# Optimization experiments

Measured on AMD Instinct MI355X. Metric: run time of the kernel, lower is better.

The kernel has to match this reference:

```python
import jax, jax.numpy as jnp
import numpy as np

EPS = 1e-5

def causal_conv1d(x, w, b, groups=1):
    # x: [B,C,L], w: [O, C//groups, K]; left-pad K-1 => causal, length preserved
    k = w.shape[-1]
    x = jnp.pad(x, ((0, 0), (0, 0), (k - 1, 0)))
    y = jax.lax.conv_general_dilated(x, w, (1,), 'VALID',
        dimension_numbers=('NCH', 'OIH', 'NCH'), feature_group_count=groups)
    return y + b[None, :, None]

def bn_eval(x, g, b):
    # BatchNorm1d eval with init running stats (mean=0, var=1)
    scale = g / jnp.sqrt(1.0 + EPS)
    return x * scale[None, :, None] + b[None, :, None]

def maxpool1d(x, k):
    B, C, L = x.shape
    return x.reshape(B, C, L // k, k).max(-1)

def mamba2_layer(u, Wi, cw, cb, dt_bias, A_log, Dh, norm_w, Wo):
    Bb, L, _ = u.shape
    H = dt_bias.shape[0]
    d_inner = norm_w.shape[0]
    P = d_inner // H
    conv_dim = cw.shape[0]
    N = (conv_dim - d_inner) // 2
    zxbcdt = u @ Wi                                   # [B,L,2*d_inner+2N+H]
    z = zxbcdt[..., :d_inner]
    xBC = zxbcdt[..., d_inner:d_inner + conv_dim]
    dt = zxbcdt[..., d_inner + conv_dim:]
    xBC = causal_conv1d(xBC.swapaxes(1, 2), cw[:, None, :], cb, groups=conv_dim)
    xBC = jax.nn.silu(xBC).swapaxes(1, 2)             # [B,L,conv_dim]
    xs = xBC[..., :d_inner].reshape(Bb, L, H, P)
    Bm = xBC[..., d_inner:d_inner + N]                # [B,L,N] (ngroups=1)
    Cm = xBC[..., d_inner + N:]                       # [B,L,N]
    dt = jax.nn.softplus(dt + dt_bias)                # [B,L,H]
    dA = jnp.exp(dt * (-jnp.exp(A_log)))              # [B,L,H]
    dtx = dt[..., None] * xs                          # [B,L,H,P]
    def step(h, inp):
        dA_t, dtx_t, B_t, C_t = inp
        h = h * dA_t[:, :, None, None] + dtx_t[..., None] * B_t[:, None, None, :]
        y = jnp.einsum('bhpn,bn->bhp', h, C_t)
        return h, y
    h0 = jnp.zeros((Bb, H, P, N), u.dtype)
    _, ys = jax.lax.scan(step, h0, (dA.swapaxes(0, 1), dtx.swapaxes(0, 1),
                                    Bm.swapaxes(0, 1), Cm.swapaxes(0, 1)))
    y = ys.swapaxes(0, 1) + Dh[None, None, :, None] * xs
    y = y.reshape(Bb, L, d_inner)
    y = y * jax.nn.silu(z)                            # gate then RMSNorm (norm_before_gate=False)
    y = y * jax.lax.rsqrt(jnp.mean(y * y, axis=-1, keepdims=True) + EPS) * norm_w
    return y @ Wo

def forward(x, idx, patch_w, patch_b, conv_w, conv_b, bn_g, bn_b,
            cls_token, pos_embed, Wi, cw, cb, dt_bias, A_log, Dh,
            norm_w, Wo, ln_g, ln_b, fc_w, fc_b):
    # PatchEmbed: Conv2d kernel (patch_size,1) on [B,1,patch_size,L] -> [B,E,L]
    h = jnp.einsum('bpl,ep->bel', x[:, 0], patch_w) + patch_b[None, :, None]
    # CausalCNN (eval mode: dropout = identity)
    h = jax.nn.relu(bn_eval(causal_conv1d(h, conv_w[0], conv_b[0]), bn_g[0], bn_b[0]))
    h = jax.nn.relu(bn_eval(causal_conv1d(h, conv_w[1], conv_b[1]), bn_g[1], bn_b[1]))
    h = maxpool1d(h, 3)
    h = jax.nn.relu(bn_eval(causal_conv1d(h, conv_w[2], conv_b[2]), bn_g[2], bn_b[2]))
    h = jax.nn.relu(bn_eval(causal_conv1d(h, conv_w[3], conv_b[3]), bn_g[3], bn_b[3]))
    h = maxpool1d(h, 2)
    h = h.swapaxes(1, 2)                              # [B, num_patches, E]
    h = h + pos_embed[:, 1:, :]
    cls = cls_token + pos_embed[:, :1, :]
    h = jnp.concatenate([jnp.broadcast_to(cls, (h.shape[0], 1, h.shape[2])), h], axis=1)
    def block(carry, p):
        return carry + mamba2_layer(carry, *p), None
    h, _ = jax.lax.scan(block, h, (Wi, cw, cb, dt_bias, A_log, Dh, norm_w, Wo))
    mu = h.mean(-1, keepdims=True)
    var = ((h - mu) ** 2).mean(-1, keepdims=True)
    h = (h - mu) * jax.lax.rsqrt(var + EPS) * ln_g + ln_b
    h = h[:, 1:, :]                                   # drop cls
    agg = idx // 6                                    # aggregate_idx
    mask = (jnp.arange(h.shape[1])[None, :] <= agg[:, None]).astype(h.dtype)
    pooled = (h * mask[..., None]).sum(1) / (agg + 1).astype(h.dtype)[:, None]
    return pooled @ fc_w + fc_b

def _sincos_pos_embed(E, L):
    pos = np.arange(L, dtype=np.float32)
    omega = 1.0 / 10000 ** (np.arange(E // 2, dtype=np.float32) / (E / 2.0))
    out = pos[:, None] * omega[None, :]
    emb = np.concatenate([np.sin(out), np.cos(out)], axis=1)
    emb = np.concatenate([np.zeros((1, E), np.float32), emb], axis=0)  # cls row
    return jnp.asarray(emb)[None]

def setup_inputs() -> dict:
    key = jax.random.key(0)
    ks = jax.random.split(key, 12)
    B, E, Lm, Psz = 16, 256, 12288, 8
    depth, H, N, d_inner, K = 8, 8, 128, 512, 4
    conv_dim = d_inner + 2 * N        # 768
    dproj = 2 * d_inner + 2 * N + H   # 1288
    NC = 100
    NP = Lm // 6                      # 2048 patches
    f32 = jnp.float32
    dt0 = jax.random.uniform(ks[2], (depth, H), f32, 0.001, 0.1)
    return dict(
        x=jax.random.normal(ks[0], (B, 1, Psz, Lm), f32),
        idx=jax.random.randint(ks[1], (B,), 0, Lm),
        patch_w=jax.random.normal(ks[3], (E, Psz), f32) * 0.1,
        patch_b=jnp.zeros((E,), f32),
        conv_w=jax.random.normal(ks[4], (4, E, E, 5), f32) * 0.02,
        conv_b=jnp.zeros((4, E), f32),
        bn_g=jnp.ones((4, E), f32), bn_b=jnp.zeros((4, E), f32),
        cls_token=jax.random.normal(ks[5], (1, 1, E), f32) * 0.02,
        pos_embed=_sincos_pos_embed(E, NP),
        Wi=jax.random.normal(ks[6], (depth, E, dproj), f32) * 0.06,
        cw=jax.random.normal(ks[7], (depth, conv_dim, K), f32) * 0.2,
        cb=jnp.zeros((depth, conv_dim), f32),
        dt_bias=dt0 + jnp.log(-jnp.expm1(-dt0)),  # inverse softplus of dt
        A_log=jnp.log(jax.random.uniform(ks[8], (depth, H), f32, 1.0, 16.0)),
        Dh=jnp.ones((depth, H), f32),
        norm_w=jnp.ones((depth, d_inner), f32),
        Wo=jax.random.normal(ks[9], (depth, d_inner, E), f32) * 0.04,
        ln_g=jnp.ones((E,), f32), ln_b=jnp.zeros((E,), f32),
        fc_w=jax.random.normal(ks[10], (E, NC), f32) * 0.05,
        fc_b=jnp.zeros((NC,), f32),
    )

def reference(x, idx, patch_w, patch_b, conv_w, conv_b, bn_g, bn_b,
              cls_token, pos_embed, Wi, cw, cb, dt_bias, A_log, Dh,
              norm_w, Wo, ln_g, ln_b, fc_w, fc_b):
    return forward(x, idx, patch_w, patch_b, conv_w, conv_b, bn_g, bn_b,
                   cls_token, pos_embed, Wi, cw, cb, dt_bias, A_log, Dh,
                   norm_w, Wo, ln_g, ln_b, fc_w, fc_b)
```

## Files before the change

kernel.cpp:

```cpp
#include <hip/hip_runtime.h>
#include <cstdint>
#include <cstddef>

#define EPSF 1e-5f

typedef unsigned short u16;
typedef __attribute__((ext_vector_type(8))) short short8v;
typedef __attribute__((ext_vector_type(4))) float f32x4;

static __device__ __forceinline__ u16 f2bf(float f) {
  union { float f; unsigned u; } v; v.f = f;
  unsigned r = v.u + 0x7fffu + ((v.u >> 16) & 1u);
  return (u16)(r >> 16);
}
static __device__ __forceinline__ float bf2f(u16 h) {
  union { unsigned u; float f; } v; v.u = ((unsigned)h) << 16;
  return v.f;
}

__global__ void k_wconv(const float* __restrict__ src, u16* __restrict__ dst) {
  int i = blockIdx.x * 256 + threadIdx.x;
  if (i >= 4 * 256 * 256 * 5) return;
  int k = i % 5, r = i / 5;
  int ci = r & 255; r >>= 8;
  int co = r & 255; int l = r >> 8;
  dst[(((size_t)l * 256 + co) * 5 + k) * 256 + ci] = f2bf(src[i]);
}
__global__ void k_wti(const float* __restrict__ src, u16* __restrict__ dst) {
  int i = blockIdx.x * 256 + threadIdx.x;
  if (i >= 8 * 1288 * 256) return;
  int k = i & 255; int r = i >> 8;
  int n = r % 1288; int l = r / 1288;
  dst[i] = f2bf(src[((size_t)l * 256 + k) * 1288 + n]);
}
__global__ void k_wto(const float* __restrict__ src, u16* __restrict__ dst) {
  int i = blockIdx.x * 256 + threadIdx.x;
  if (i >= 8 * 256 * 512) return;
  int k = i & 511; int r = i >> 9;
  int n = r & 255; int l = r >> 8;
  dst[i] = f2bf(src[((size_t)l * 512 + k) * 256 + n]);
}

__global__ __launch_bounds__(256) void k_patchm(const float* __restrict__ x, const float* __restrict__ pw,
                                                const float* __restrict__ pb, u16* __restrict__ outb) {
  __shared__ float xs[8][64];
  const int l0 = blockIdx.x * 64;
  const int b = blockIdx.y;
  const int tid = threadIdx.x;
  const float* xb = x + (size_t)b * 8 * 12288;
  for (int q = tid; q < 512; q += 256) {
    int p = q >> 6, ll = q & 63;
    xs[p][ll] = xb[(size_t)p * 12288 + l0 + ll];
  }
  __syncthreads();
  float pwr[8];
#pragma unroll
  for (int p = 0; p < 8; ++p) pwr[p] = pw[tid * 8 + p];
  const float bias = pb[tid];
  u16* ob = outb + ((size_t)b * 12288 + l0) * 256 + tid;
  for (int ll = 0; ll < 64; ++ll) {
    float acc = bias;
#pragma unroll
    for (int p = 0; p < 8; ++p) acc += xs[p][ll] * pwr[p];
    ob[(size_t)ll * 256] = f2bf(acc);
  }
}

template <int P2>
__global__ __launch_bounds__(256) void k_convm(const u16* __restrict__ in, const u16* __restrict__ wbf,
                                               const float* __restrict__ cbias, const float* __restrict__ bng,
                                               const float* __restrict__ bnb, u16* __restrict__ outb, int L) {
  __shared__ u16 Xs[132 * 40];
  __shared__ u16 Ws[64 * 168];
  const int l0 = blockIdx.x * 128;
  const int co0 = blockIdx.y * 64;
  const int b = blockIdx.z;
  const int tid = threadIdx.x;
  const int w = tid >> 6, l = tid & 63;
  const int mhalf = (w >> 1) * 64, nhalf = (w & 1) * 32;
  const u16* inb = in + (size_t)b * L * 256;
  f32x4 acc[4][2] = {};
  for (int ci0 = 0; ci0 < 256; ci0 += 32) {
    __syncthreads();
    for (int q = tid; q < 528; q += 256) {
      int row = q >> 2, coff = (q & 3) * 8;
      int gl = l0 - 4 + row;
      short8v v = {};
      if (gl >= 0) v = *(const short8v*)(inb + (size_t)gl * 256 + ci0 + coff);
      *(short8v*)(Xs + row * 40 + coff) = v;
    }
    for (int q = tid; q < 1280; q += 256) {
      int co = q / 20, rem = q % 20, k = rem >> 2, coff = (rem & 3) * 8;
      *(short8v*)(Ws + co * 168 + k * 32 + coff) =
          *(const short8v*)(wbf + ((size_t)(co0 + co) * 5 + k) * 256 + ci0 + coff);
    }
    __syncthreads();
    const int koff = (l >> 4) * 8;
    const int arow = mhalf + (l & 15);
    const int bro0 = (nhalf + (l & 15)) * 168;
    const int bro1 = (nhalf + 16 + (l & 15)) * 168;
#pragma unroll
    for (int k = 0; k < 5; ++k) {
      short8v b0 = *(const short8v*)(Ws + bro0 + k * 32 + koff);
      short8v b1 = *(const short8v*)(Ws + bro1 + k * 32 + koff);
#pragma unroll
      for (int mi = 0; mi < 4; ++mi) {
        short8v a = *(const short8v*)(Xs + (arow + mi * 16 + k) * 40 + koff);
        acc[mi][0] = __builtin_amdgcn_mfma_f32_16x16x32_bf16(a, b0, acc[mi][0], 0, 0, 0);
        acc[mi][1] = __builtin_amdgcn_mfma_f32_16x16x32_bf16(a, b1, acc[mi][1], 0, 0, 0);
      }
    }
  }
  const float scn = rsqrtf(1.f + EPSF);
  if constexpr (!P2) {
    u16* outbb = outb + (size_t)b * L * 256;
#pragma unroll
    for (int ni = 0; ni < 2; ++ni) {
      int co = co0 + nhalf + ni * 16 + (l & 15);
      float alpha = bng[co] * scn;
      float beta = cbias[co] * alpha + bnb[co];
#pragma unroll
      for (int mi = 0; mi < 4; ++mi)
#pragma unroll
        for (int r = 0; r < 4; ++r) {
          int row = l0 + mhalf + mi * 16 + (l >> 4) * 4 + r;
          float v = acc[mi][ni][r] * alpha + beta;
          outbb[(size_t)row * 256 + co] = f2bf(fmaxf(v, 0.f));
        }
    }
  } else {
    const int Lo = L >> 1;
    u16* outbb = outb + (size_t)b * Lo * 256;
#pragma unroll
    for (int ni = 0; ni < 2; ++ni) {
      int co = co0 + nhalf + ni * 16 + (l & 15);
      float alpha = bng[co] * scn;
      float beta = cbias[co] * alpha + bnb[co];
#pragma unroll
      for (int mi = 0; mi < 4; ++mi) {
        int base = l0 + mhalf + mi * 16 + (l >> 4) * 4;
        float vv[4];
#pragma unroll
        for (int r = 0; r < 4; ++r) vv[r] = fmaxf(acc[mi][ni][r] * alpha + beta, 0.f);
#pragma unroll
        for (int pr = 0; pr < 2; ++pr) {
          float m2 = fmaxf(vv[2 * pr], vv[2 * pr + 1]);
          int orow = (base >> 1) + pr;
          outbb[(size_t)orow * 256 + co] = f2bf(m2);
        }
      }
    }
  }
}

__global__ void k_mpb(const u16* __restrict__ in, u16* __restrict__ out, int Lout, int kp, size_t total) {
  size_t i = (size_t)blockIdx.x * 256 + threadIdx.x;
  if (i >= total) return;
  size_t c = i & 255;
  size_t rest = i >> 8;
  size_t lo = rest % (size_t)Lout;
  size_t b = rest / (size_t)Lout;
  const u16* p = in + (b * (size_t)Lout * kp + lo * kp) * 256 + c;
  float m = bf2f(p[0]);
  for (int j = 1; j < kp; ++j) m = fmaxf(m, bf2f(p[(size_t)j * 256]));
  out[i] = f2bf(m);
}

__global__ __launch_bounds__(256) void k_asmb(const u16* __restrict__ in, const float* __restrict__ pos,
                                              const float* __restrict__ cls, float* __restrict__ uc,
                                              u16* __restrict__ ubc) {
  int t = blockIdx.x;
  int b = blockIdx.y;
  int e = threadIdx.x;
  float v;
  if (t == 0)
    v = cls[e] + pos[e];
  else
    v = bf2f(in[((size_t)b * 2048 + (t - 1)) * 256 + e]) + pos[(size_t)t * 256 + e];
  size_t o = ((size_t)b * 2049 + t) * 256 + e;
  uc[o] = v;
  ubc[o] = f2bf(v);
}

template <int MODE>
__global__ __launch_bounds__(256) void k_gemmm(const u16* __restrict__ A, const u16* __restrict__ BT,
                                               u16* __restrict__ OB, float* __restrict__ DT,
                                               float* __restrict__ C, u16* __restrict__ ubf,
                                               int M, int N, int K) {
  __shared__ u16 As[128 * 40];
  __shared__ u16 Bs[64 * 40];
  const int n0 = blockIdx.x * 64;
  const int m0 = blockIdx.y * 128;
  const int tid = threadIdx.x;
  const int w = tid >> 6, l = tid & 63;
  const int mhalf = (w >> 1) * 64, nhalf = (w & 1) * 32;
  f32x4 acc[4][2] = {};
  for (int k0 = 0; k0 < K; k0 += 32) {
    __syncthreads();
    for (int q = tid; q < 512; q += 256) {
      int row = q >> 2, koff = (q & 3) * 8;
      short8v v = {};
      if (m0 + row < M) v = *(const short8v*)(A + (size_t)(m0 + row) * K + k0 + koff);
      *(short8v*)(As + row * 40 + koff) = v;
    }
    {
      int row = tid >> 2, koff = (tid & 3) * 8;
      short8v v = {};
      if (n0 + row < N) v = *(const short8v*)(BT + (size_t)(n0 + row) * K + k0 + koff);
      *(short8v*)(Bs + row * 40 + koff) = v;
    }
    __syncthreads();
    const int koff = (l >> 4) * 8;
    short8v b0 = *(const short8v*)(Bs + (nhalf + (l & 15)) * 40 + koff);
    short8v b1 = *(const short8v*)(Bs + (nhalf + 16 + (l & 15)) * 40 + koff);
#pragma unroll
    for (int mi = 0; mi < 4; ++mi) {
      short8v a = *(const short8v*)(As + (mhalf + mi * 16 + (l & 15)) * 40 + koff);
      acc[mi][0] = __builtin_amdgcn_mfma_f32_16x16x32_bf16(a, b0, acc[mi][0], 0, 0, 0);
      acc[mi][1] = __builtin_amdgcn_mfma_f32_16x16x32_bf16(a, b1, acc[mi][1], 0, 0, 0);
    }
  }
#pragma unroll
  for (int mi = 0; mi < 4; ++mi)
#pragma unroll
    for (int r = 0; r < 4; ++r) {
      int m = m0 + mhalf + mi * 16 + (l >> 4) * 4 + r;
      if (m >= M) continue;
#pragma unroll
      for (int ni = 0; ni < 2; ++ni) {
        int n = n0 + nhalf + ni * 16 + (l & 15);
        if (n >= N) continue;
        float v = acc[mi][ni][r];
        if constexpr (MODE == 0) {
          if (n < 1280) OB[(size_t)m * 1280 + n] = f2bf(v);
          else DT[(size_t)m * 8 + (n - 1280)] = v;
        } else {
          float vv = C[(size_t)m * N + n] + v;
          C[(size_t)m * N + n] = vv;
          ubf[(size_t)m * N + n] = f2bf(vv);
        }
      }
    }
}

__global__ __launch_bounds__(256) void k_dw(const u16* __restrict__ zxb, const float* __restrict__ dtr,
                                            const float* __restrict__ cw, const float* __restrict__ cb,
                                            const float* __restrict__ dtbias, const float* __restrict__ al,
                                            u16* __restrict__ xBCb, float* __restrict__ dtb,
                                            float* __restrict__ ldb) {
  const int bx = blockIdx.x;
  const int t0 = blockIdx.y * 16;
  const int b = blockIdx.z;
  if (bx == 3) {
    int h = threadIdx.x & 7, ro = threadIdx.x >> 3;
    if (ro < 16) {
      int r = t0 + ro;
      if (r < 2049) {
        float v = dtr[((size_t)b * 2049 + r) * 8 + h] + dtbias[h];
        float d = (v > 20.f) ? v : log1pf(expf(v));
        size_t o = ((size_t)b * 2049 + r) * 8 + h;
        dtb[o] = d;
        ldb[o] = -expf(al[h]) * d;
      }
    }
    return;
  }
  int c = bx * 256 + threadIdx.x;
  const u16* col = zxb + ((size_t)b * 2049) * 1280 + 512 + c;
  float cw0 = cw[c * 4 + 0], cw1 = cw[c * 4 + 1], cw2 = cw[c * 4 + 2], cw3 = cw[c * 4 + 3];
  const float bias = cb[c];
  float w0 = 0.f, w1 = 0.f, w2 = 0.f;
  if (t0 - 3 >= 0) w0 = bf2f(col[(size_t)(t0 - 3) * 1280]);
  if (t0 - 2 >= 0) w1 = bf2f(col[(size_t)(t0 - 2) * 1280]);
  if (t0 - 1 >= 0) w2 = bf2f(col[(size_t)(t0 - 1) * 1280]);
  int tend = t0 + 16; if (tend > 2049) tend = 2049;
  u16* ob = xBCb + ((size_t)b * 2049) * 768 + c;
  for (int t = t0; t < tend; ++t) {
    float v = bf2f(col[(size_t)t * 1280]);
    float acc = bias + w0 * cw0 + w1 * cw1 + w2 * cw2 + v * cw3;
    float sig = 1.f / (1.f + expf(-acc));
    ob[(size_t)t * 768] = f2bf(acc * sig);
    w0 = w1; w1 = w2; w2 = v;
  }
}

__global__ __launch_bounds__(256) void k_ssd_intra(const u16* __restrict__ xBCb,
                                                   const float* __restrict__ dtg,
                                                   const float* __restrict__ ldg,
                                                   u16* __restrict__ ybuf,
                                                   u16* __restrict__ sc,
                                                   float* __restrict__ dtot) {
  const int L = 2049;
  const int c = blockIdx.x, h = blockIdx.y, b = blockIdx.z;
  const int tid = threadIdx.x;
  const int w = tid >> 6, l = tid & 63;
  const int t0 = c * 128;
  int qc = L - t0; if (qc > 128) qc = 128;

  __shared__ u16 R1[128 * 136];
  __shared__ u16 R2[128 * 136];
  __shared__ float dt_s[128], Lc_s[128];

  const u16* xb = xBCb + ((size_t)b * L) * 768;

  if (tid < 64) {
    int i2 = tid * 2;
    float a0 = 0.f, a1 = 0.f, d0 = 0.f, d1 = 0.f;
    if (i2 < qc) { size_t r = ((size_t)b * L + t0 + i2) * 8 + h; a0 = ldg[r]; d0 = dtg[r]; }
    if (i2 + 1 < qc) { size_t r = ((size_t)b * L + t0 + i2 + 1) * 8 + h; a1 = ldg[r]; d1 = dtg[r]; }
    dt_s[i2] = d0; dt_s[i2 + 1] = d1;
    float v = a0 + a1;
#pragma unroll
    for (int dlt = 1; dlt < 64; dlt <<= 1) {
      float t = __shfl_up(v, dlt, 64);
      if (tid >= dlt) v += t;
    }
    Lc_s[i2 + 1] = v;
    Lc_s[i2] = v - a1;
  }

  for (int q = tid; q < 2048; q += 256) {
    int row = q >> 4, off = (q & 15) * 8;
    short8v vb = {}, vc = {};
    if (row < qc) {
      const u16* src = xb + (size_t)(t0 + row) * 768;
      vb = *(const short8v*)(src + 512 + off);
      vc = *(const short8v*)(src + 640 + off);
    }
    *(short8v*)(R1 + row * 136 + off) = vb;
    *(short8v*)(R2 + row * 136 + off) = vc;
  }
  __syncthreads();

  const int wm = (w >> 1) * 64, wn = (w & 1) * 64;
  f32x4 g[4][4] = {};
  const bool skipG = (wm < wn);
  if (!skipG) {
#pragma unroll
    for (int ks = 0; ks < 4; ++ks) {
      const int koff = ks * 32 + (l >> 4) * 8;
      short8v bf[4];
#pragma unroll
      for (int ni = 0; ni < 4; ++ni)
        bf[ni] = *(const short8v*)(R1 + (wn + ni * 16 + (l & 15)) * 136 + koff);
#pragma unroll
      for (int mi = 0; mi < 4; ++mi) {
        short8v a = *(const short8v*)(R2 + (wm + mi * 16 + (l & 15)) * 136 + koff);
#pragma unroll
        for (int ni = 0; ni < 4; ++ni)
          g[mi][ni] = __builtin_amdgcn_mfma_f32_16x16x32_bf16(a, bf[ni], g[mi][ni], 0, 0, 0);
      }
    }
  }
  __syncthreads();

#pragma unroll
  for (int mi = 0; mi < 4; ++mi)
#pragma unroll
    for (int r = 0; r < 4; ++r) {
      int t = wm + mi * 16 + (l >> 4) * 4 + r;
      float lct = Lc_s[t];
#pragma unroll
      for (int ni = 0; ni < 4; ++ni) {
        int s = wn + ni * 16 + (l & 15);
        float v = 0.f;
        if (s <= t) v = __expf(lct - Lc_s[s]) * dt_s[s] * g[mi][ni][r];
        R2[t * 136 + s] = f2bf(v);
      }
    }
  for (int q = tid; q < 1024; q += 256) {
    int s = q >> 3, pv = (q & 7) * 8;
    short8v v = {};
    if (s < qc) v = *(const short8v*)(xb + (size_t)(t0 + s) * 768 + h * 64 + pv);
#pragma unroll
    for (int j = 0; j < 8; ++j) R1[(pv + j) * 136 + s] = (u16)v[j];
  }
  if (tid == 0) dtot[((size_t)b * 8 + h) * 17 + c] = __expf(Lc_s[qc - 1]);
  __syncthreads();

  {
    const int wmy = (w >> 1) * 64, wny = (w & 1) * 32;
    f32x4 ya[4][2] = {};
#pragma unroll
    for (int ks = 0; ks < 4; ++ks) {
      const int koff = ks * 32 + (l >> 4) * 8;
      short8v b0 = *(const short8v*)(R1 + (wny + (l & 15)) * 136 + koff);
      short8v b1 = *(const short8v*)(R1 + (wny + 16 + (l & 15)) * 136 + koff);
#pragma unroll
      for (int mi = 0; mi < 4; ++mi) {
        short8v a = *(const short8v*)(R2 + (wmy + mi * 16 + (l & 15)) * 136 + koff);
        ya[mi][0] = __builtin_amdgcn_mfma_f32_16x16x32_bf16(a, b0, ya[mi][0], 0, 0, 0);
        ya[mi][1] = __builtin_amdgcn_mfma_f32_16x16x32_bf16(a, b1, ya[mi][1], 0, 0, 0);
      }
    }
    u16* yb = ybuf + ((size_t)b * L + t0) * 512 + h * 64;
#pragma unroll
    for (int mi = 0; mi < 4; ++mi)
#pragma unroll
      for (int r = 0; r < 4; ++r) {
        int t = wmy + mi * 16 + (l >> 4) * 4 + r;
        if (t >= qc) continue;
#pragma unroll
        for (int ni = 0; ni < 2; ++ni) {
          int p = wny + ni * 16 + (l & 15);
          yb[(size_t)t * 512 + p] = f2bf(ya[mi][ni][r]);
        }
      }
  }
  __syncthreads();

  {
    const float Lend = Lc_s[qc - 1];
    for (int q = tid; q < 8192; q += 256) {
      int p = q >> 7, s = q & 127;
      float w2 = __expf(Lend - Lc_s[s]) * dt_s[s];
      R1[p * 136 + s] = f2bf(bf2f(R1[p * 136 + s]) * w2);
    }
    for (int q = tid; q < 2048; q += 256) {
      int s = q >> 4, nv = (q & 15) * 8;
      short8v v = {};
      if (s < qc) v = *(const short8v*)(xb + (size_t)(t0 + s) * 768 + 512 + nv);
#pragma unroll
      for (int j = 0; j < 8; ++j) R2[(nv + j) * 136 + s] = (u16)v[j];
    }
  }
  __syncthreads();

  {
    const int wms = (w & 1) * 32, wns = (w >> 1) * 64;
    f32x4 sa[2][4] = {};
#pragma unroll
    for (int ks = 0; ks < 4; ++ks) {
      const int koff = ks * 32 + (l >> 4) * 8;
      short8v a0 = *(const short8v*)(R1 + (wms + (l & 15)) * 136 + koff);
      short8v a1 = *(const short8v*)(R1 + (wms + 16 + (l & 15)) * 136 + koff);
#pragma unroll
      for (int ni = 0; ni < 4; ++ni) {
        short8v bb = *(const short8v*)(R2 + (wns + ni * 16 + (l & 15)) * 136 + koff);
        sa[0][ni] = __builtin_amdgcn_mfma_f32_16x16x32_bf16(a0, bb, sa[0][ni], 0, 0, 0);
        sa[1][ni] = __builtin_amdgcn_mfma_f32_16x16x32_bf16(a1, bb, sa[1][ni], 0, 0, 0);
      }
    }
    u16* scp = sc + (((size_t)b * 8 + h) * 17 + c) * 8192;
#pragma unroll
    for (int mi = 0; mi < 2; ++mi)
#pragma unroll
      for (int r = 0; r < 4; ++r) {
        int p = wms + mi * 16 + (l >> 4) * 4 + r;
#pragma unroll
        for (int ni = 0; ni < 4; ++ni) {
          int n = wns + ni * 16 + (l & 15);
          scp[p * 128 + n] = f2bf(sa[mi][ni][r]);
        }
      }
  }
}

__global__ __launch_bounds__(256) void k_ssd_scan(u16* __restrict__ sc, const float* __restrict__ dtot,
                                                  int nbh) {
  int gid = blockIdx.x * 256 + threadIdx.x;
  int bh = gid >> 13;
  if (bh >= nbh) return;
  int elem = gid & 8191;
  u16* base = sc + (size_t)bh * 17 * 8192 + elem;
  const float* dtp = dtot + (size_t)bh * 17;
  float hc = 0.f;
#pragma unroll
  for (int cc = 0; cc < 17; ++cc) {
    float D = dtp[cc];
    float v = bf2f(base[(size_t)cc * 8192]);
    base[(size_t)cc * 8192] = f2bf(hc);
    hc = hc * D + v;
  }
}

__global__ __launch_bounds__(256) void k_ssd_inter(const u16* __restrict__ xBCb,
                                                   const float* __restrict__ ldg,
                                                   const u16* __restrict__ sc,
                                                   const float* __restrict__ Dh,
                                                   u16* __restrict__ ybuf) {
  const int L = 2049;
  const int c = blockIdx.x, h = blockIdx.y, b = blockIdx.z;
  const int tid = threadIdx.x;
  const int w = tid >> 6, l = tid & 63;
  const int t0 = c * 128;
  int qc = L - t0; if (qc > 128) qc = 128;

  __shared__ u16 Cs[128 * 136];
  __shared__ u16 H0[64 * 136];
  __shared__ float Lc_s[128];

  const u16* xb = xBCb + ((size_t)b * L) * 768;

  if (tid < 64) {
    int i2 = tid * 2;
    float a0 = 0.f, a1 = 0.f;
    if (i2 < qc) a0 = ldg[((size_t)b * L + t0 + i2) * 8 + h];
    if (i2 + 1 < qc) a1 = ldg[((size_t)b * L + t0 + i2 + 1) * 8 + h];
    float v = a0 + a1;
#pragma unroll
    for (int dlt = 1; dlt < 64; dlt <<= 1) {
      float t = __shfl_up(v, dlt, 64);
      if (tid >= dlt) v += t;
    }
    Lc_s[i2 + 1] = v;
    Lc_s[i2] = v - a1;
  }
  for (int q = tid; q < 2048; q += 256) {
    int row = q >> 4, off = (q & 15) * 8;
    short8v vc = {};
    if (row < qc) vc = *(const short8v*)(xb + (size_t)(t0 + row) * 768 + 640 + off);
    *(short8v*)(Cs + row * 136 + off) = vc;
  }
  {
    const u16* hp = sc + (((size_t)b * 8 + h) * 17 + c) * 8192;
    for (int q = tid; q < 1024; q += 256) {
      int p = q >> 4, nv = (q & 15) * 8;
      *(short8v*)(H0 + p * 136 + nv) = *(const short8v*)(hp + p * 128 + nv);
    }
  }
  __syncthreads();

  const int wm = (w >> 1) * 64, wn = (w & 1) * 32;
  f32x4 acc[4][2] = {};
#pragma unroll
  for (int ks = 0; ks < 4; ++ks) {
    const int koff = ks * 32 + (l >> 4) * 8;
    short8v b0 = *(const short8v*)(H0 + (wn + (l & 15)) * 136 + koff);
    short8v b1 = *(const short8v*)(H0 + (wn + 16 + (l & 15)) * 136 + koff);
#pragma unroll
    for (int mi = 0; mi < 4; ++mi) {
      short8v a = *(const short8v*)(Cs + (wm + mi * 16 + (l & 15)) * 136 + koff);
      acc[mi][0] = __builtin_amdgcn_mfma_f32_16x16x32_bf16(a, b0, acc[mi][0], 0, 0, 0);
      acc[mi][1] = __builtin_amdgcn_mfma_f32_16x16x32_bf16(a, b1, acc[mi][1], 0, 0, 0);
    }
  }
  const float DD = Dh[h];
  u16* yb = ybuf + ((size_t)b * L + t0) * 512 + h * 64;
#pragma unroll
  for (int mi = 0; mi < 4; ++mi)
#pragma unroll
    for (int r = 0; r < 4; ++r) {
      int t = wm + mi * 16 + (l >> 4) * 4 + r;
      if (t >= qc) continue;
      float e = __expf(Lc_s[t]);
#pragma unroll
      for (int ni = 0; ni < 2; ++ni) {
        int p = wn + ni * 16 + (l & 15);
        float xs = bf2f(xb[(size_t)(t0 + t) * 768 + h * 64 + p]);
        float old = bf2f(yb[(size_t)t * 512 + p]);
        yb[(size_t)t * 512 + p] = f2bf(old + e * acc[mi][ni][r] + DD * xs);
      }
    }
}

__global__ __launch_bounds__(256) void k_gaterms(const u16* __restrict__ ybuf, const u16* __restrict__ zxb,
                                                 const float* __restrict__ nw, u16* __restrict__ y2,
                                                 int Mc) {
  int row = blockIdx.x * 4 + (threadIdx.x >> 6);
  if (row >= Mc) return;
  int lane = threadIdx.x & 63;
  const u16* yr = ybuf + (size_t)row * 512 + lane * 8;
  const u16* zr = zxb + (size_t)row * 1280 + lane * 8;
  short8v yv8 = *(const short8v*)yr;
  short8v zv8 = *(const short8v*)zr;
  float g[8];
  float ss = 0.f;
#pragma unroll
  for (int j = 0; j < 8; ++j) {
    float yv = bf2f((u16)yv8[j]);
    float zv = bf2f((u16)zv8[j]);
    float sig = 1.f / (1.f + expf(-zv));
    float gg = yv * zv * sig;
    g[j] = gg;
    ss += gg * gg;
  }
#pragma unroll
  for (int off = 32; off > 0; off >>= 1) ss += __shfl_xor(ss, off);
  float r = rsqrtf(ss * (1.f / 512.f) + EPSF);
#pragma unroll
  for (int j = 0; j < 8; ++j)
    y2[(size_t)row * 512 + lane * 8 + j] = f2bf(g[j] * r * nw[lane * 8 + j]);
}

__global__ __launch_bounds__(256) void k_ln(const float* __restrict__ u, const float* __restrict__ g,
                                            const float* __restrict__ bb, float* __restrict__ out) {
  int rid = blockIdx.x * 4 + (threadIdx.x >> 6);
  int lane = threadIdx.x & 63;
  int b = rid >> 11;
  int t = (rid & 2047) + 1;
  const float* ur = u + ((size_t)b * 2049 + t) * 256 + lane * 4;
  float v[4];
  float s1 = 0.f, s2 = 0.f;
#pragma unroll
  for (int j = 0; j < 4; ++j) {
    v[j] = ur[j];
    s1 += v[j];
    s2 += v[j] * v[j];
  }
#pragma unroll
  for (int off = 32; off > 0; off >>= 1) {
    s1 += __shfl_xor(s1, off);
    s2 += __shfl_xor(s2, off);
  }
  float mu = s1 * (1.f / 256.f);
  float var = s2 * (1.f / 256.f) - mu * mu;
  float rs = rsqrtf(var + EPSF);
  float* orow = out + ((size_t)b * 2048 + (t - 1)) * 256 + lane * 4;
#pragma unroll
  for (int j = 0; j < 4; ++j) orow[j] = (v[j] - mu) * rs * g[lane * 4 + j] + bb[lane * 4 + j];
}

__global__ __launch_bounds__(256) void k_pp(const float* __restrict__ hln, const int* __restrict__ idx,
                                            float* __restrict__ part) {
  int ch = blockIdx.x;
  int b = blockIdx.y;
  int e = threadIdx.x;
  int agg = idx[b] / 6;
  int t0 = ch * 64;
  int tend = agg + 1 - t0;
  if (tend > 64) tend = 64;
  float s = 0.f;
  for (int i = 0; i < tend; ++i) s += hln[((size_t)b * 2048 + t0 + i) * 256 + e];
  part[((size_t)b * 32 + ch) * 256 + e] = s;
}

__global__ __launch_bounds__(256) void k_fc(const float* __restrict__ part, const int* __restrict__ idx,
                                            const float* __restrict__ fw, const float* __restrict__ fb,
                                            float* __restrict__ out) {
  __shared__ float pooled[256];
  int b = blockIdx.x;
  int tid = threadIdx.x;
  float s = 0.f;
#pragma unroll
  for (int ch = 0; ch < 32; ++ch) s += part[((size_t)b * 32 + ch) * 256 + tid];
  pooled[tid] = s;
  __syncthreads();
  if (tid < 100) {
    int agg = idx[b] / 6;
    float inv = 1.f / (float)(agg + 1);
    float acc = 0.f;
    for (int e = 0; e < 256; ++e) acc += pooled[e] * fw[e * 100 + tid];
    out[b * 100 + tid] = acc * inv + fb[tid];
  }
}

extern "C" void kernel_launch(void* const* d_in, const int* in_sizes, int n_in,
                              void* d_out, int out_size, void* d_ws, size_t ws_size,
                              hipStream_t stream) {
  (void)in_sizes; (void)n_in; (void)out_size;
  const float* x        = (const float*)d_in[0];
  const int*   idx      = (const int*)d_in[1];
  const float* patch_w  = (const float*)d_in[2];
  const float* patch_b  = (const float*)d_in[3];
  const float* conv_w   = (const float*)d_in[4];
  const float* conv_b   = (const float*)d_in[5];
  const float* bn_g     = (const float*)d_in[6];
  const float* bn_b     = (const float*)d_in[7];
  const float* cls_tok  = (const float*)d_in[8];
  const float* pos_emb  = (const float*)d_in[9];
  const float* Wi       = (const float*)d_in[10];
  const float* cw       = (const float*)d_in[11];
  const float* cb       = (const float*)d_in[12];
  const float* dt_bias  = (const float*)d_in[13];
  const float* A_log    = (const float*)d_in[14];
  const float* Dh       = (const float*)d_in[15];
  const float* norm_w   = (const float*)d_in[16];
  const float* Wo       = (const float*)d_in[17];
  const float* ln_g     = (const float*)d_in[18];
  const float* ln_b     = (const float*)d_in[19];
  const float* fc_w     = (const float*)d_in[20];
  const float* fc_b     = (const float*)d_in[21];
  float* out = (float*)d_out;
  float* ws = (float*)d_ws;

  auto need = [](size_t cb) {
    size_t Rsz = cb * 3753496ull;
    if (Rsz < 8388608ull) Rsz = 8388608ull;
    return (8392704ull + Rsz + 4096 + 1318912 + 524288 + 655360 + 131072 + cb * 262272ull) * 4ull;
  };
  size_t CB = 16;
  while (CB > 1 && ws_size < need(CB)) CB >>= 1;
  const int NCHUNK = (int)(16 / CB);
  const int Mc = (int)(CB * 2049);

  size_t Rsz = CB * 3753496ull;
  if (Rsz < 8388608ull) Rsz = 8388608ull;

  float* u   = ws;
  float* R   = u + 8392704;
  u16*  zxb  = (u16*)R;
  float* dtr = R + CB * 1311360;
  float* dtb = dtr + CB * 16392;
  float* ldb = dtb + CB * 16392;
  float* afterldb = ldb + CB * 16392;
  u16*  xBCb = (u16*)afterldb;
  u16*  ybufb = (u16*)(afterldb + CB * 786816);
  u16*  y2bf = (u16*)(afterldb + CB * 786816 + CB * 524544);
  u16*  scb = (u16*)(afterldb + CB * 786816 + CB * 524544 + CB * 524544);
  u16* fA = (u16*)R;
  u16* fB = (u16*)(R + CB * 1572864);
  float* hln = R;
  float* dtot = R + Rsz;
  u16*  WiT  = (u16*)(dtot + 4096);
  u16*  WoT  = (u16*)((float*)WiT + 1318912);
  u16*  wbf  = (u16*)((float*)WoT + 524288);
  float* ppar = (float*)wbf + 655360;
  u16*  u_bf = (u16*)(ppar + 131072);

  k_wconv<<<dim3((4 * 256 * 256 * 5 + 255) / 256), 256, 0, stream>>>(conv_w, wbf);
  k_wti<<<dim3((8 * 1288 * 256 + 255) / 256), 256, 0, stream>>>(Wi, WiT);
  k_wto<<<dim3((8 * 256 * 512 + 255) / 256), 256, 0, stream>>>(Wo, WoT);

  const unsigned gy = (unsigned)((Mc + 127) / 128);

  for (int bc = 0; bc < NCHUNK; ++bc) {
    const float* xc = x + (size_t)bc * CB * 8 * 12288;
    float* uc = u + (size_t)bc * CB * 2049 * 256;

    k_patchm<<<dim3(192, (unsigned)CB), 256, 0, stream>>>(xc, patch_w, patch_b, fA);
    k_convm<0><<<dim3(96, 4, (unsigned)CB), 256, 0, stream>>>(fA, wbf + 0 * 327680, conv_b + 0, bn_g + 0, bn_b + 0, fB, 12288);
    k_convm<0><<<dim3(96, 4, (unsigned)CB), 256, 0, stream>>>(fB, wbf + 1 * 327680, conv_b + 256, bn_g + 256, bn_b + 256, fA, 12288);
    {
      size_t tot = CB * 4096 * 256;
      k_mpb<<<dim3((unsigned)((tot + 255) / 256)), 256, 0, stream>>>(fA, fB, 4096, 3, tot);
    }
    k_convm<0><<<dim3(32, 4, (unsigned)CB), 256, 0, stream>>>(fB, wbf + 2 * 327680, conv_b + 512, bn_g + 512, bn_b + 512, fA, 4096);
    k_convm<1><<<dim3(32, 4, (unsigned)CB), 256, 0, stream>>>(fA, wbf + 3 * 327680, conv_b + 768, bn_g + 768, bn_b + 768, fB, 4096);
    k_asmb<<<dim3(2049, (unsigned)CB), 256, 0, stream>>>(fB, pos_emb, cls_tok, uc, u_bf);

    for (int l = 0; l < 8; ++l) {
      const u16* WiTl = WiT + (size_t)l * 1288 * 256;
      const u16* WoTl = WoT + (size_t)l * 256 * 512;
      const float* cwl  = cw + (size_t)l * 768 * 4;
      const float* cbl  = cb + (size_t)l * 768;
      const float* dtbl = dt_bias + l * 8;
      const float* all  = A_log + l * 8;
      const float* dhl  = Dh + l * 8;
      const float* nwl  = norm_w + (size_t)l * 512;

      k_gemmm<0><<<dim3(21, gy), 256, 0, stream>>>(u_bf, WiTl, zxb, dtr, nullptr, nullptr, Mc, 1288, 256);
      k_dw<<<dim3(4, 129, (unsigned)CB), 256, 0, stream>>>(zxb, dtr, cwl, cbl, dtbl, all, xBCb, dtb, ldb);
      k_ssd_intra<<<dim3(17, 8, (unsigned)CB), 256, 0, stream>>>(xBCb, dtb, ldb, ybufb, scb, dtot);
      k_ssd_scan<<<dim3((unsigned)(CB * 8 * 32)), 256, 0, stream>>>(scb, dtot, (int)(CB * 8));
      k_ssd_inter<<<dim3(17, 8, (unsigned)CB), 256, 0, stream>>>(xBCb, ldb, scb, dhl, ybufb);
      k_gaterms<<<dim3((unsigned)((Mc + 3) / 4)), 256, 0, stream>>>(ybufb, zxb, nwl, y2bf, Mc);
      k_gemmm<1><<<dim3(4, gy), 256, 0, stream>>>(y2bf, WoTl, nullptr, nullptr, uc, u_bf, Mc, 256, 512);
    }
  }

  k_ln<<<dim3(8192), 256, 0, stream>>>(u, ln_g, ln_b, hln);
  k_pp<<<dim3(32, 16), 256, 0, stream>>>(hln, idx, ppar);
  k_fc<<<dim3(16), 256, 0, stream>>>(ppar, idx, fc_w, fc_b, out);
}
```

Before: 3.667 ms.

## Compute head-shared C·B^T Gram matrix once per chunk instead of per head

Moves the C·Bᵀ MFMA product into a new kernel, because with a single group this product is identical for all 8 heads. The new kernel writes it once per (chunk, batch) as fp32 into a global scratch buffer that reuses the y2bf region. k_ssd_intra then reads it from global memory instead of loading B/C and running the MFMAs itself. This removes the redundant per-head matmuls and B/C loads, at the cost of an extra launch and a sizeable fp32 global write/read round-trip through cache.

```diff
diff --git a/kernel.cpp b/kernel.cpp
--- a/kernel.cpp
+++ b/kernel.cpp
@@ -284,9 +284,68 @@
   }
 }
 
+__global__ __launch_bounds__(256) void k_ssd_g(const u16* __restrict__ xBCb,
+                                               float* __restrict__ G) {
+  const int L = 2049;
+  const int c = blockIdx.x, b = blockIdx.y;
+  const int tid = threadIdx.x;
+  const int w = tid >> 6, l = tid & 63;
+  const int t0 = c * 128;
+  int qc = L - t0; if (qc > 128) qc = 128;
+
+  __shared__ u16 R1[128 * 136];
+  __shared__ u16 R2[128 * 136];
+
+  const u16* xb = xBCb + ((size_t)b * L) * 768;
+  for (int q = tid; q < 2048; q += 256) {
+    int row = q >> 4, off = (q & 15) * 8;
+    short8v vb = {}, vc = {};
+    if (row < qc) {
+      const u16* src = xb + (size_t)(t0 + row) * 768;
+      vb = *(const short8v*)(src + 512 + off);
+      vc = *(const short8v*)(src + 640 + off);
+    }
+    *(short8v*)(R1 + row * 136 + off) = vb;
+    *(short8v*)(R2 + row * 136 + off) = vc;
+  }
+  __syncthreads();
+
+  const int wm = (w >> 1) * 64, wn = (w & 1) * 64;
+  if (wm < wn) return;
+  f32x4 g[4][4] = {};
+#pragma unroll
+  for (int ks = 0; ks < 4; ++ks) {
+    const int koff = ks * 32 + (l >> 4) * 8;
+    short8v bf[4];
+#pragma unroll
+    for (int ni = 0; ni < 4; ++ni)
+      bf[ni] = *(const short8v*)(R1 + (wn + ni * 16 + (l & 15)) * 136 + koff);
+#pragma unroll
+    for (int mi = 0; mi < 4; ++mi) {
+      short8v a = *(const short8v*)(R2 + (wm + mi * 16 + (l & 15)) * 136 + koff);
+#pragma unroll
+      for (int ni = 0; ni < 4; ++ni)
+        g[mi][ni] = __builtin_amdgcn_mfma_f32_16x16x32_bf16(a, bf[ni], g[mi][ni], 0, 0, 0);
+    }
+  }
+  float* Gp = G + ((size_t)b * 17 + c) * 16384;
+#pragma unroll
+  for (int mi = 0; mi < 4; ++mi)
+#pragma unroll
+    for (int r = 0; r < 4; ++r) {
+      int t = wm + mi * 16 + (l >> 4) * 4 + r;
+#pragma unroll
+      for (int ni = 0; ni < 4; ++ni) {
+        int s = wn + ni * 16 + (l & 15);
+        Gp[t * 128 + s] = g[mi][ni][r];
+      }
+    }
+}
+
 __global__ __launch_bounds__(256) void k_ssd_intra(const u16* __restrict__ xBCb,
                                                    const float* __restrict__ dtg,
                                                    const float* __restrict__ ldg,
+                                                   const float* __restrict__ G,
                                                    u16* __restrict__ ybuf,
                                                    u16* __restrict__ sc,
                                                    float* __restrict__ dtot) {
@@ -319,55 +378,6 @@
     Lc_s[i2] = v - a1;
   }
 
-  for (int q = tid; q < 2048; q += 256) {
-    int row = q >> 4, off = (q & 15) * 8;
-    short8v vb = {}, vc = {};
-    if (row < qc) {
-      const u16* src = xb + (size_t)(t0 + row) * 768;
-      vb = *(const short8v*)(src + 512 + off);
-      vc = *(const short8v*)(src + 640 + off);
-    }
-    *(short8v*)(R1 + row * 136 + off) = vb;
-    *(short8v*)(R2 + row * 136 + off) = vc;
-  }
-  __syncthreads();
-
-  const int wm = (w >> 1) * 64, wn = (w & 1) * 64;
-  f32x4 g[4][4] = {};
-  const bool skipG = (wm < wn);
-  if (!skipG) {
-#pragma unroll
-    for (int ks = 0; ks < 4; ++ks) {
-      const int koff = ks * 32 + (l >> 4) * 8;
-      short8v bf[4];
-#pragma unroll
-      for (int ni = 0; ni < 4; ++ni)
-        bf[ni] = *(const short8v*)(R1 + (wn + ni * 16 + (l & 15)) * 136 + koff);
-#pragma unroll
-      for (int mi = 0; mi < 4; ++mi) {
-        short8v a = *(const short8v*)(R2 + (wm + mi * 16 + (l & 15)) * 136 + koff);
-#pragma unroll
-        for (int ni = 0; ni < 4; ++ni)
-          g[mi][ni] = __builtin_amdgcn_mfma_f32_16x16x32_bf16(a, bf[ni], g[mi][ni], 0, 0, 0);
-      }
-    }
-  }
-  __syncthreads();
-
-#pragma unroll
-  for (int mi = 0; mi < 4; ++mi)
-#pragma unroll
-    for (int r = 0; r < 4; ++r) {
-      int t = wm + mi * 16 + (l >> 4) * 4 + r;
-      float lct = Lc_s[t];
-#pragma unroll
-      for (int ni = 0; ni < 4; ++ni) {
-        int s = wn + ni * 16 + (l & 15);
-        float v = 0.f;
-        if (s <= t) v = __expf(lct - Lc_s[s]) * dt_s[s] * g[mi][ni][r];
-        R2[t * 136 + s] = f2bf(v);
-      }
-    }
   for (int q = tid; q < 1024; q += 256) {
     int s = q >> 3, pv = (q & 7) * 8;
     short8v v = {};
@@ -375,6 +385,24 @@
 #pragma unroll
     for (int j = 0; j < 8; ++j) R1[(pv + j) * 136 + s] = (u16)v[j];
   }
+  __syncthreads();
+
+  const float* Gp = G + ((size_t)b * 17 + c) * 16384;
+  const int wm = (w >> 1) * 64, wn = (w & 1) * 64;
+#pragma unroll
+  for (int mi = 0; mi < 4; ++mi)
+#pragma unroll
+    for (int r = 0; r < 4; ++r) {
+      int t = wm + mi * 16 + (l >> 4) * 4 + r;
+      float lct = Lc_s[t];
+#pragma unroll
+      for (int ni = 0; ni < 4; ++ni) {
+        int s = wn + ni * 16 + (l & 15);
+        float v = 0.f;
+        if (s <= t) v = __expf(lct - Lc_s[s]) * dt_s[s] * Gp[t * 128 + s];
+        R2[t * 136 + s] = f2bf(v);
+      }
+    }
   if (tid == 0) dtot[((size_t)b * 8 + h) * 17 + c] = __expf(Lc_s[qc - 1]);
   __syncthreads();
 
@@ -697,6 +725,7 @@
   u16*  xBCb = (u16*)afterldb;
   u16*  ybufb = (u16*)(afterldb + CB * 786816);
   u16*  y2bf = (u16*)(afterldb + CB * 786816 + CB * 524544);
+  float* Gbuf = afterldb + CB * 786816 + CB * 524544;
   u16*  scb = (u16*)(afterldb + CB * 786816 + CB * 524544 + CB * 524544);
   u16* fA = (u16*)R;
   u16* fB = (u16*)(R + CB * 1572864);
@@ -741,7 +770,8 @@
 
       k_gemmm<0><<<dim3(21, gy), 256, 0, stream>>>(u_bf, WiTl, zxb, dtr, nullptr, nullptr, Mc, 1288, 256);
       k_dw<<<dim3(4, 129, (unsigned)CB), 256, 0, stream>>>(zxb, dtr, cwl, cbl, dtbl, all, xBCb, dtb, ldb);
-      k_ssd_intra<<<dim3(17, 8, (unsigned)CB), 256, 0, stream>>>(xBCb, dtb, ldb, ybufb, scb, dtot);
+      k_ssd_g<<<dim3(17, (unsigned)CB), 256, 0, stream>>>(xBCb, Gbuf);
+      k_ssd_intra<<<dim3(17, 8, (unsigned)CB), 256, 0, stream>>>(xBCb, dtb, ldb, Gbuf, ybufb, scb, dtot);
       k_ssd_scan<<<dim3((unsigned)(CB * 8 * 32)), 256, 0, stream>>>(scb, dtot, (int)(CB * 8));
       k_ssd_inter<<<dim3(17, 8, (unsigned)CB), 256, 0, stream>>>(xBCb, ldb, scb, dhl, ybufb);
       k_gaterms<<<dim3((unsigned)((Mc + 3) / 4)), 256, 0, stream>>>(ybufb, zxb, nwl, y2bf, Mc);
```

Result: slower. 4.041 ms (+10.2%).
